# Performance work log

Hardware: AMD Instinct MI355X
Metric: run time of the kernel (lower is better)

Reference implementation:

```python
import jax, jax.numpy as jnp
import numpy as np

B, L, E, H = 4, 4096, 1024, 16
DH = E // H          # 64 head dim
R, M, P = 1, 8, 16   # quadrature nodes, prf features, poly sketch dim
EPS = 1e-6
C = 2.0 + EPS


def setup_inputs() -> dict:
    key = jax.random.key(0)
    ks = jax.random.split(key, 10)
    x = jax.random.normal(ks[0], (B, L, E), dtype=jnp.float32)
    qkv_w = jax.random.normal(ks[1], (E, 3 * E), dtype=jnp.float32) * 0.02
    qkv_b = jnp.zeros((3 * E,), dtype=jnp.float32)
    out_w = jax.random.normal(ks[2], (E, E), dtype=jnp.float32) * 0.02
    out_b = jnp.zeros((E,), dtype=jnp.float32)
    omega = jax.random.normal(ks[3], (R, H, DH, M), dtype=jnp.float32)
    ts_hash1 = jax.random.randint(ks[4], (DH,), 0, P)
    ts_sign1 = jax.random.randint(ks[5], (DH,), 0, 2) * 2 - 1
    ts_hash2 = jax.random.randint(ks[6], (DH,), 0, P)
    ts_sign2 = jax.random.randint(ks[7], (DH,), 0, 2) * 2 - 1
    # laggauss(1): node=1.0, weight=1.0
    quad_nodes = jnp.array([1.0], dtype=jnp.float32) / C
    quad_weights = jnp.array([1.0], dtype=jnp.float32) / C
    return {"x": x, "qkv_w": qkv_w, "qkv_b": qkv_b, "out_w": out_w,
            "out_b": out_b, "omega": omega, "quad_nodes": quad_nodes,
            "quad_weights": quad_weights, "ts_hash1": ts_hash1,
            "ts_sign1": ts_sign1, "ts_hash2": ts_hash2, "ts_sign2": ts_sign2}


def _safe_normalize(x, eps=1e-6):
    norm = jnp.linalg.norm(x, axis=-1, keepdims=True)
    return x / jnp.clip(norm, eps)


def _count_sketch(x, h, s):
    # x: (B,H,L,DH); h,s: (DH,) int
    vals = x * s.astype(x.dtype)
    Mhot = jax.nn.one_hot(h, P, dtype=x.dtype)  # (DH, P)
    return jnp.dot(vals, Mhot)                  # (B,H,L,P)


def _poly_tensor_sketch(x, h1, s1, h2, s2):
    cs1 = _count_sketch(x, h1, s1)
    cs2 = _count_sketch(x, h2, s2)
    f1 = jnp.fft.rfft(cs1, axis=-1)
    f2 = jnp.fft.rfft(cs2, axis=-1)
    ts = jnp.fft.irfft(f1 * f2, n=P, axis=-1)
    return ts / jnp.sqrt(float(P))


def _prf_features(x, omega, quad_nodes):
    proj = jnp.einsum('bhld,rhdm->rbhlm', x, omega)
    s_vals = quad_nodes.reshape(-1, 1, 1, 1, 1)
    sqrt_2s = jnp.sqrt(2.0 * jnp.clip(s_vals, 0.0))
    exp_arg = jnp.clip(proj * sqrt_2s - s_vals, -10.0, 10.0)
    return jnp.exp(exp_arg) / jnp.sqrt(float(M))


def reference(x, qkv_w, qkv_b, out_w, out_b, omega, quad_nodes, quad_weights,
              ts_hash1, ts_sign1, ts_hash2, ts_sign2):
    qkv = x @ qkv_w + qkv_b
    q, k, v = jnp.split(qkv, 3, axis=-1)
    q = q.reshape(B, L, H, DH).transpose(0, 2, 1, 3)
    k = k.reshape(B, L, H, DH).transpose(0, 2, 1, 3)
    v = v.reshape(B, L, H, DH).transpose(0, 2, 1, 3)

    q_norm = _safe_normalize(q)
    k_norm = _safe_normalize(k)

    q_poly = _poly_tensor_sketch(q_norm, ts_hash1, ts_sign1, ts_hash2, ts_sign2)
    k_poly = _poly_tensor_sketch(k_norm, ts_hash1, ts_sign1, ts_hash2, ts_sign2)
    q_prf = _prf_features(q_norm, omega, quad_nodes)
    k_prf = _prf_features(k_norm, omega, quad_nodes)

    sq_w = jnp.sqrt(jnp.clip(quad_weights.reshape(-1, 1, 1, 1, 1), 0.0))
    q_prf = q_prf * sq_w
    k_prf = k_prf * sq_w

    q_fuse = jnp.einsum('bhlp,rbhlm->bhlrpm', q_poly, q_prf).reshape(B, H, L, -1)
    k_fuse = jnp.einsum('bhlp,rbhlm->bhlrpm', k_poly, k_prf).reshape(B, H, L, -1)

    kv = jnp.einsum('bhlf,bhld->bhfd', k_fuse, v)
    context = jnp.einsum('bhlf,bhfd->bhld', q_fuse, kv)
    k_sum = k_fuse.sum(axis=2)                              # (B,H,F)
    norm = jnp.einsum('bhlf,bhf->bhl', q_fuse, k_sum)
    output = context / jnp.clip(norm, 0.0001)[..., None]

    output = output.transpose(0, 2, 1, 3).reshape(B, L, E)
    return output @ out_w + out_b
```

## Files before the change

### kernel.cpp

```cpp
#include <hip/hip_runtime.h>

typedef unsigned short u16;
typedef __attribute__((ext_vector_type(8))) short bfrag8;
typedef __attribute__((ext_vector_type(4))) float f32x4;

__device__ __forceinline__ float b2f(u16 u){ union { unsigned ui; float f; } v; v.ui = ((unsigned)u) << 16; return v.f; }
__device__ __forceinline__ u16 f2b(float f){ union { float f; unsigned ui; } v; v.f = f; unsigned r = (v.ui + 0x7FFF + ((v.ui >> 16) & 1)) >> 16; return (u16)r; }

__device__ __forceinline__ void gl_lds16(const u16* g, u16* l){
  __builtin_amdgcn_global_load_lds(
      (const __attribute__((address_space(1))) unsigned*)g,
      (__attribute__((address_space(3))) unsigned*)l, 16, 0, 0);
}

__global__ __launch_bounds__(256) void zero_f32(float* p, int n){
  int i = blockIdx.x*256 + threadIdx.x;
  if (i < n) p[i] = 0.f;
}

__global__ __launch_bounds__(256) void split_x(const float* __restrict__ x,
    u16* __restrict__ xh, u16* __restrict__ xl){
  size_t i = ((size_t)blockIdx.x*256 + threadIdx.x) * 8;
  float v[8];
  *(float4*)v       = *(const float4*)(x + i);
  *(float4*)(v + 4) = *(const float4*)(x + i + 4);
  u16 h[8], l[8];
  #pragma unroll
  for (int j = 0; j < 8; ++j){ u16 a = f2b(v[j]); h[j] = a; l[j] = f2b(v[j] - b2f(a)); }
  *(uint4*)(xh + i) = *(uint4*)h;
  *(uint4*)(xl + i) = *(uint4*)l;
}

__global__ __launch_bounds__(256) void transpose_split(const float* __restrict__ W,
    u16* __restrict__ Th, u16* __restrict__ Tl, int K, int N){
  __shared__ float tile[32][33];
  int bx = blockIdx.x * 32, by = blockIdx.y * 32;
  int tx = threadIdx.x & 31, ty = threadIdx.x >> 5;
  #pragma unroll
  for (int i = 0; i < 32; i += 8) tile[ty+i][tx] = W[(size_t)(by+ty+i)*N + bx+tx];
  __syncthreads();
  #pragma unroll
  for (int i = 0; i < 32; i += 8){
    float v = tile[tx][ty+i];
    u16 h = f2b(v);
    Th[(size_t)(bx+ty+i)*K + by+tx] = h;
    Tl[(size_t)(bx+ty+i)*K + by+tx] = f2b(v - b2f(h));
  }
}

__global__ __launch_bounds__(256) void transpose_f2b(const float* __restrict__ W, u16* __restrict__ Wt, int K, int N){
  __shared__ u16 tile[32][33];
  int bx = blockIdx.x * 32, by = blockIdx.y * 32;
  int tx = threadIdx.x & 31, ty = threadIdx.x >> 5;
  #pragma unroll
  for (int i = 0; i < 32; i += 8) tile[ty+i][tx] = f2b(W[(size_t)(by+ty+i)*N + bx+tx]);
  __syncthreads();
  #pragma unroll
  for (int i = 0; i < 32; i += 8) Wt[(size_t)(bx+ty+i)*K + by+tx] = tile[tx][ty+i];
}

template<int NPROD>
__global__ __launch_bounds__(256) void gemm_planes(
    const u16* __restrict__ Ah, const u16* __restrict__ Al, int lda,
    const u16* __restrict__ Bh, const u16* __restrict__ Bl, int bn_off,
    const float* __restrict__ bias,
    float* __restrict__ Cq, float* __restrict__ Ck, u16* __restrict__ Cv, int K)
{
  constexpr int NS = (NPROD==3) ? 2 : 1;
  __shared__ __align__(16) u16 As[2*NS*4096];
  __shared__ __align__(16) u16 Bs[2*NS*4096];
  int tid = threadIdx.x, lane = tid & 63, wave = tid >> 6;
  int wm = wave >> 1, wn = wave & 1;
  int bm = blockIdx.y * 128, bn = blockIdx.x * 128;
  f32x4 acc[4][4];
  #pragma unroll
  for (int i=0;i<4;i++)
    #pragma unroll
    for (int j=0;j<4;j++)
      #pragma unroll
      for (int r=0;r<4;r++) acc[i][j][r] = 0.f;
  int mr = lane & 15, g = lane >> 4;
  int srow = (wave & 1)*64 + lane;
  int kc1 = (wave >> 1)*8;
  int kc2 = kc1 + 16;
  const u16* gA0 = Ah + (size_t)(bm + srow)*lda;
  const u16* gA1 = Al + (size_t)(bm + srow)*lda;
  const u16* gB0 = Bh + (size_t)(bn_off + bn + srow)*K;
  const u16* gB1 = Bl + (size_t)(bn_off + bn + srow)*K;
  u16* As0 = As;  u16* As1 = As + NS*4096;
  u16* Bs0 = Bs;  u16* Bs1 = Bs + NS*4096;

#define STG_P(AD, BD, KO) { \
    gl_lds16(gA0 + (KO) + kc1, (AD) + wave*512); \
    gl_lds16(gA0 + (KO) + kc2, (AD) + (wave+4)*512); \
    gl_lds16(gB0 + (KO) + kc1, (BD) + wave*512); \
    gl_lds16(gB0 + (KO) + kc2, (BD) + (wave+4)*512); \
    if constexpr (NS > 1){ \
      gl_lds16(gA1 + (KO) + kc1, (AD) + 4096 + wave*512); \
      gl_lds16(gA1 + (KO) + kc2, (AD) + 4096 + (wave+4)*512); \
      gl_lds16(gB1 + (KO) + kc1, (BD) + 4096 + wave*512); \
      gl_lds16(gB1 + (KO) + kc2, (BD) + 4096 + (wave+4)*512); } }

#define MMACC(sa,sb) \
    { _Pragma("unroll") for (int i=0;i<4;i++){ _Pragma("unroll") for (int j=0;j<4;j++){ \
        acc[i][j] = __builtin_amdgcn_mfma_f32_16x16x32_bf16(af[sa][i], bf[sb][j], acc[i][j], 0, 0, 0); } } }

#define CMP_P(AS, BS) { \
    bfrag8 af[NS][4], bf[NS][4]; \
    _Pragma("unroll") \
    for (int s=0;s<NS;s++){ \
      _Pragma("unroll") \
      for (int i=0;i<4;i++) af[s][i] = *(const bfrag8*)((AS) + s*4096 + g*1024 + (wm*64 + i*16 + mr)*8); \
      _Pragma("unroll") \
      for (int j=0;j<4;j++) bf[s][j] = *(const bfrag8*)((BS) + s*4096 + g*1024 + (wn*64 + j*16 + mr)*8); } \
    if constexpr (NPROD == 3){ MMACC(0,1) MMACC(1,0) } \
    MMACC(0,0) }

  STG_P(As0, Bs0, 0)
  __syncthreads();
  for (int k0 = 0; k0 < K; k0 += 64) {
    STG_P(As1, Bs1, k0 + 32)
    CMP_P(As0, Bs0)
    __syncthreads();
    if (k0 + 64 < K) { STG_P(As0, Bs0, k0 + 64) }
    CMP_P(As1, Bs1)
    __syncthreads();
  }
#undef STG_P
#undef CMP_P
#undef MMACC

  #pragma unroll
  for (int i=0;i<4;i++){
    #pragma unroll
    for (int j=0;j<4;j++){
      int col = bn_off + bn + wn*64 + j*16 + (lane & 15);
      float bv = bias[col];
      #pragma unroll
      for (int r=0;r<4;r++){
        int row = bm + wm*64 + i*16 + (lane>>4)*4 + r;
        float val = acc[i][j][r] + bv;
        if (col < 1024)      Cq[(size_t)row*1024 + col]        = val;
        else if (col < 2048) Ck[(size_t)row*1024 + (col-1024)] = val;
        else                 Cv[(size_t)row*1024 + (col-2048)] = f2b(val);
      }
    }
  }
}

__global__ __launch_bounds__(256) void gemm_b16(const u16* __restrict__ A, int lda,
    const u16* __restrict__ Bt, const float* __restrict__ bias, float* __restrict__ C, int N, int K)
{
  __shared__ __align__(16) u16 As[2*4096];
  __shared__ __align__(16) u16 Bs[2*4096];
  int tid = threadIdx.x, lane = tid & 63, wave = tid >> 6;
  int wm = wave >> 1, wn = wave & 1;
  int bm = blockIdx.y * 128, bn = blockIdx.x * 128;
  f32x4 acc[4][4];
  #pragma unroll
  for (int i=0;i<4;i++)
    #pragma unroll
    for (int j=0;j<4;j++)
      #pragma unroll
      for (int r=0;r<4;r++) acc[i][j][r] = 0.f;
  int mr = lane & 15, g = lane >> 4;
  int srow = (wave & 1)*64 + lane;
  int kc1 = (wave >> 1)*8, kc2 = kc1 + 16;
  const u16* gA = A  + (size_t)(bm + srow)*lda;
  const u16* gB = Bt + (size_t)(bn + srow)*K;
  u16* As0 = As;  u16* As1 = As + 4096;
  u16* Bs0 = Bs;  u16* Bs1 = Bs + 4096;

#define STG_B(AD, BD, KO) { \
    gl_lds16(gA + (KO) + kc1, (AD) + wave*512); \
    gl_lds16(gA + (KO) + kc2, (AD) + (wave+4)*512); \
    gl_lds16(gB + (KO) + kc1, (BD) + wave*512); \
    gl_lds16(gB + (KO) + kc2, (BD) + (wave+4)*512); }

#define CMP_B(AS, BS) { \
    bfrag8 af[4], bf[4]; \
    _Pragma("unroll") \
    for (int i=0;i<4;i++) af[i] = *(const bfrag8*)((AS) + g*1024 + (wm*64 + i*16 + mr)*8); \
    _Pragma("unroll") \
    for (int j=0;j<4;j++) bf[j] = *(const bfrag8*)((BS) + g*1024 + (wn*64 + j*16 + mr)*8); \
    _Pragma("unroll") \
    for (int i=0;i<4;i++){ \
      _Pragma("unroll") \
      for (int j=0;j<4;j++) \
        acc[i][j] = __builtin_amdgcn_mfma_f32_16x16x32_bf16(af[i], bf[j], acc[i][j], 0, 0, 0); } }

  STG_B(As0, Bs0, 0)
  __syncthreads();
  for (int k0 = 0; k0 < K; k0 += 64) {
    STG_B(As1, Bs1, k0 + 32)
    CMP_B(As0, Bs0)
    __syncthreads();
    if (k0 + 64 < K) { STG_B(As0, Bs0, k0 + 64) }
    CMP_B(As1, Bs1)
    __syncthreads();
  }
#undef STG_B
#undef CMP_B

  #pragma unroll
  for (int i=0;i<4;i++){
    #pragma unroll
    for (int j=0;j<4;j++){
      int col = bn + wn*64 + j*16 + (lane & 15);
      float bv = bias[col];
      #pragma unroll
      for (int r=0;r<4;r++){
        int row = bm + wm*64 + i*16 + (lane>>4)*4 + r;
        C[(size_t)row*N + col] = acc[i][j][r] + bv;
      }
    }
  }
}

struct __align__(16) ConsT { int b1; float sg1; int b2; float sg2; };

#define FEATS_COMPUTE(TILE, TOKA)                                                \
  float sq = 0.f;                                                                \
  _Pragma("unroll")                                                              \
  for (int dd = 0; dd < 16; ++dd){ float u = TILE[(TOKA)*65 + g*16 + dd]; sq += u*u; } \
  sq += __shfl_xor(sq, 16); sq += __shfl_xor(sq, 32);                            \
  float sc = 1.f / fmaxf(sqrtf(sq), 1e-6f);                                      \
  float cs1[16], cs2[16], pm[8];                                                 \
  _Pragma("unroll") for (int p=0;p<16;p++){ cs1[p]=0.f; cs2[p]=0.f; }            \
  _Pragma("unroll") for (int m=0;m<8;m++) pm[m]=0.f;                             \
  _Pragma("unroll")                                                              \
  for (int dd = 0; dd < 16; ++dd){                                               \
    int d = g*16 + dd;                                                           \
    float un = TILE[(TOKA)*65 + d] * sc;                                         \
    ConsT cc = cons[d];                                                          \
    float v1 = un*cc.sg1, v2 = un*cc.sg2;                                        \
    _Pragma("unroll")                                                            \
    for (int p=0;p<16;p++){ cs1[p] += (cc.b1==p)?v1:0.f; cs2[p] += (cc.b2==p)?v2:0.f; } \
    _Pragma("unroll")                                                            \
    for (int m=0;m<8;m++) pm[m] += un * oms[d*8 + m];                            \
  }                                                                              \
  _Pragma("unroll")                                                              \
  for (int p=0;p<16;p++){ cs1[p] += __shfl_xor(cs1[p],16); cs1[p] += __shfl_xor(cs1[p],32); \
                          cs2[p] += __shfl_xor(cs2[p],16); cs2[p] += __shfl_xor(cs2[p],32); } \
  _Pragma("unroll")                                                              \
  for (int m=0;m<8;m++){ pm[m] += __shfl_xor(pm[m],16); pm[m] += __shfl_xor(pm[m],32); } \
  float poly4[4];                                                                \
  _Pragma("unroll")                                                              \
  for (int pi=0;pi<4;pi++){ int p = g*4 + pi; float s = 0.f;                     \
    _Pragma("unroll") for (int a=0;a<16;a++) s += cs1[a]*cs2[(p-a)&15];          \
    poly4[pi] = s * 0.25f; }                                                     \
  float prf[8];                                                                  \
  _Pragma("unroll")                                                              \
  for (int m=0;m<8;m++){ float e = fminf(fmaxf(pm[m]*sqrt2s - s_node, -10.f), 10.f); \
    prf[m] = expf(e) * pscale; }

__global__ __launch_bounds__(256) void kfeat_kv(const float* __restrict__ kf, const u16* __restrict__ vb,
    const float* __restrict__ omega, const float* __restrict__ qn, const float* __restrict__ qw,
    const int* __restrict__ h1, const int* __restrict__ s1,
    const int* __restrict__ h2, const int* __restrict__ s2,
    float* __restrict__ kvT, float* __restrict__ ksum)
{
  __shared__ float ktile[64*65];
  __shared__ __align__(16) u16 vtile[64*64];
  __shared__ __align__(16) u16 featT[128*72];
  __shared__ float oms[64*8];
  __shared__ ConsT cons[64];
  int tid = threadIdx.x, lane = tid & 63, wave = tid >> 6;
  int bh = blockIdx.y, b = bh >> 4, h = bh & 15;
  int chunk = blockIdx.x;
  if (tid < 64) {
    ConsT c; c.b1 = h1[tid]; c.sg1 = (float)s1[tid]; c.b2 = h2[tid]; c.sg2 = (float)s2[tid];
    cons[tid] = c;
  }
  for (int i = tid; i < 512; i += 256) oms[i] = omega[h*512 + i];
  float s_node = qn[0];
  float sqrt2s = sqrtf(2.f * fmaxf(s_node, 0.f));
  float pscale = 0.35355339059327373f * sqrtf(fmaxf(qw[0], 0.f));
  int tloc = lane & 15, g = lane >> 4;
  int tokA = wave*16 + tloc;
  int wm = wave >> 1, wn = wave & 1;
  int mr = lane & 15, kq8 = (lane >> 4) * 8;
  f32x4 acc[4][2];
  #pragma unroll
  for (int i=0;i<4;i++)
    #pragma unroll
    for (int jn=0;jn<2;jn++)
      #pragma unroll
      for (int r=0;r<4;r++) acc[i][jn][r] = 0.f;
  float kacc[32];
  #pragma unroll
  for (int j=0;j<32;j++) kacc[j] = 0.f;
  for (int sub = 0; sub < 8; ++sub) {
    int base = chunk*512 + sub*64;
    __syncthreads();
    for (int idx = tid; idx < 4096; idx += 256) {
      int t = idx >> 6, d = idx & 63;
      ktile[t*65 + d] = kf[(size_t)(b*4096 + base + t)*1024 + h*64 + d];
    }
    for (int slot = tid; slot < 512; slot += 256) {
      int t = slot >> 3, o = (slot & 7) * 8;
      *(uint4*)(&vtile[t*64 + o]) = *(const uint4*)(&vb[(size_t)(b*4096 + base + t)*1024 + h*64 + o]);
    }
    __syncthreads();
    {
      FEATS_COMPUTE(ktile, tokA)
      #pragma unroll
      for (int pi=0;pi<4;pi++){
        #pragma unroll
        for (int m=0;m<8;m++){
          int f = (g*4 + pi)*8 + m;
          float v = poly4[pi]*prf[m];
          featT[f*72 + tokA] = f2b(v);
          v += __shfl_xor(v,1); v += __shfl_xor(v,2); v += __shfl_xor(v,4); v += __shfl_xor(v,8);
          if (tloc == 0) kacc[pi*8 + m] += v;
        }
      }
    }
    __syncthreads();
    #pragma unroll
    for (int k0 = 0; k0 < 64; k0 += 32) {
      bfrag8 af[4];
      #pragma unroll
      for (int i=0;i<4;i++) af[i] = *(const bfrag8*)(&featT[(wm*64 + i*16 + mr)*72 + k0 + kq8]);
      #pragma unroll
      for (int jn=0;jn<2;jn++){
        int d = wn*32 + jn*16 + mr;
        short tmp[8];
        #pragma unroll
        for (int j=0;j<8;j++) tmp[j] = (short)vtile[(k0 + kq8 + j)*64 + d];
        bfrag8 bf = *(bfrag8*)tmp;
        #pragma unroll
        for (int i=0;i<4;i++)
          acc[i][jn] = __builtin_amdgcn_mfma_f32_16x16x32_bf16(af[i], bf, acc[i][jn], 0, 0, 0);
      }
    }
  }
  #pragma unroll
  for (int i=0;i<4;i++){
    #pragma unroll
    for (int jn=0;jn<2;jn++){
      int d = wn*32 + jn*16 + (lane & 15);
      #pragma unroll
      for (int r=0;r<4;r++){
        int f = wm*64 + i*16 + (lane>>4)*4 + r;
        atomicAdd(&kvT[((size_t)bh*64 + d)*128 + f], acc[i][jn][r]);
      }
    }
  }
  if (tloc == 0){
    #pragma unroll
    for (int j=0;j<32;j++) atomicAdd(&ksum[bh*128 + g*32 + j], kacc[j]);
  }
}

__global__ __launch_bounds__(256) void qfeat_ctx(const float* __restrict__ qf,
    const float* __restrict__ omega, const float* __restrict__ qn, const float* __restrict__ qw,
    const int* __restrict__ h1, const int* __restrict__ s1,
    const int* __restrict__ h2, const int* __restrict__ s2,
    const float* __restrict__ kvT, const float* __restrict__ ksum,
    u16* __restrict__ attn)
{
  __shared__ float qtile[64*65];
  __shared__ __align__(16) u16 feat[64*136];
  __shared__ __align__(16) u16 kvsb0[64*136];
  __shared__ __align__(16) u16 kvsb1[64*136];
  __shared__ float ksums[128];
  __shared__ float nrm_s[64];
  __shared__ float oms[64*8];
  __shared__ ConsT cons[64];
  int tid = threadIdx.x, lane = tid & 63, wave = tid >> 6;
  int bh = blockIdx.y, b = bh >> 4, h = bh & 15;
  int chunk = blockIdx.x;
  if (tid < 64) {
    ConsT c; c.b1 = h1[tid]; c.sg1 = (float)s1[tid]; c.b2 = h2[tid]; c.sg2 = (float)s2[tid];
    cons[tid] = c;
  }
  for (int i = tid; i < 512; i += 256) oms[i] = omega[h*512 + i];
  for (int idx = tid; idx < 8192; idx += 256) {
    int d = idx >> 7, f = idx & 127;
    float v = kvT[((size_t)bh*64 + d)*128 + f];
    u16 b0 = f2b(v);
    kvsb0[d*136 + f] = b0;
    kvsb1[d*136 + f] = f2b(v - b2f(b0));
  }
  if (tid < 128) ksums[tid] = ksum[bh*128 + tid];
  float s_node = qn[0];
  float sqrt2s = sqrtf(2.f * fmaxf(s_node, 0.f));
  float pscale = 0.35355339059327373f * sqrtf(fmaxf(qw[0], 0.f));
  int tloc = lane & 15, g = lane >> 4;
  int tokA = wave*16 + tloc;
  int mr = lane & 15, kq8 = (lane >> 4) * 8;
  for (int sub = 0; sub < 8; ++sub) {
    int base = chunk*512 + sub*64;
    for (int idx = tid; idx < 4096; idx += 256) {
      int t = idx >> 6, d = idx & 63;
      qtile[t*65 + d] = qf[(size_t)(b*4096 + base + t)*1024 + h*64 + d];
    }
    __syncthreads();
    {
      FEATS_COMPUTE(qtile, tokA)
      float nv = 0.f;
      #pragma unroll
      for (int pi=0;pi<4;pi++){
        #pragma unroll
        for (int m=0;m<8;m++){
          int f = (g*4 + pi)*8 + m;
          float v = poly4[pi]*prf[m];
          feat[tokA*136 + f] = f2b(v);
          nv += v * ksums[f];
        }
      }
      nv += __shfl_xor(nv, 16); nv += __shfl_xor(nv, 32);
      if (lane < 16) nrm_s[tokA] = nv;
    }
    __syncthreads();
    f32x4 cacc[4];
    #pragma unroll
    for (int jn=0;jn<4;jn++)
      #pragma unroll
      for (int r=0;r<4;r++) cacc[jn][r] = 0.f;
    #pragma unroll
    for (int k0 = 0; k0 < 128; k0 += 32) {
      bfrag8 af = *(const bfrag8*)(&feat[(wave*16 + mr)*136 + k0 + kq8]);
      #pragma unroll
      for (int jn=0;jn<4;jn++){
        int d = jn*16 + mr;
        bfrag8 b0 = *(const bfrag8*)(&kvsb0[d*136 + k0 + kq8]);
        cacc[jn] = __builtin_amdgcn_mfma_f32_16x16x32_bf16(af, b0, cacc[jn], 0, 0, 0);
        bfrag8 b1 = *(const bfrag8*)(&kvsb1[d*136 + k0 + kq8]);
        cacc[jn] = __builtin_amdgcn_mfma_f32_16x16x32_bf16(af, b1, cacc[jn], 0, 0, 0);
      }
    }
    #pragma unroll
    for (int jn=0;jn<4;jn++){
      int d = jn*16 + (lane & 15);
      #pragma unroll
      for (int r=0;r<4;r++){
        int row = (lane>>4)*4 + r;
        float nrm = nrm_s[wave*16 + row];
        int tok = base + wave*16 + row;
        attn[(size_t)(b*4096 + tok)*2048 + h*64 + d] = f2b(cacc[jn][r] / fmaxf(nrm, 1e-4f));
      }
    }
  }
}

extern "C" void kernel_launch(void* const* d_in, const int* in_sizes, int n_in,
                              void* d_out, int out_size, void* d_ws, size_t ws_size,
                              hipStream_t stream)
{
  const float* x     = (const float*)d_in[0];
  const float* qkv_w = (const float*)d_in[1];
  const float* qkv_b = (const float*)d_in[2];
  const float* out_w = (const float*)d_in[3];
  const float* out_b = (const float*)d_in[4];
  const float* omega = (const float*)d_in[5];
  const float* qn    = (const float*)d_in[6];
  const float* qw    = (const float*)d_in[7];
  const int* h1 = (const int*)d_in[8];
  const int* s1 = (const int*)d_in[9];
  const int* h2 = (const int*)d_in[10];
  const int* s2 = (const int*)d_in[11];

  const size_t SZ_Q  = (size_t)16384*1024*4;
  const size_t SZ_K  = (size_t)16384*1024*4;
  const size_t SZ_V  = (size_t)16384*1024*2;
  const size_t SZ_XH = (size_t)16384*1024*2;
  const size_t SZ_XL = (size_t)16384*1024*2;
  const size_t SZ_WH = (size_t)3072*1024*2;
  const size_t SZ_WL = (size_t)3072*1024*2;
  const size_t SZ_W2 = (size_t)1024*1024*2;
  const size_t SZ_KV = (size_t)64*64*128*4;
  char* ws = (char*)d_ws;
  float* qf  = (float*)ws;
  float* kf  = (float*)(ws + SZ_Q);
  u16*   vb  = (u16*)  (ws + SZ_Q + SZ_K);
  u16*   xh  = (u16*)  (ws + SZ_Q + SZ_K + SZ_V);
  u16*   xl  = (u16*)  (ws + SZ_Q + SZ_K + SZ_V + SZ_XH);
  u16*   wTh = (u16*)  (ws + SZ_Q + SZ_K + SZ_V + SZ_XH + SZ_XL);
  u16*   wTl = (u16*)  (ws + SZ_Q + SZ_K + SZ_V + SZ_XH + SZ_XL + SZ_WH);
  u16*   wT2 = (u16*)  (ws + SZ_Q + SZ_K + SZ_V + SZ_XH + SZ_XL + SZ_WH + SZ_WL);
  float* kvT = (float*)(ws + SZ_Q + SZ_K + SZ_V + SZ_XH + SZ_XL + SZ_WH + SZ_WL + SZ_W2);
  float* ksp = (float*)(ws + SZ_Q + SZ_K + SZ_V + SZ_XH + SZ_XL + SZ_WH + SZ_WL + SZ_W2 + SZ_KV);

  int nz = (int)((SZ_KV + (size_t)64*128*4) / 4);
  zero_f32<<<(nz+255)/256, 256, 0, stream>>>(kvT, nz);
  split_x<<<(16384*1024/8)/256, 256, 0, stream>>>(x, xh, xl);
  transpose_split<<<dim3(3072/32, 1024/32), 256, 0, stream>>>(qkv_w, wTh, wTl, 1024, 3072);
  transpose_f2b<<<dim3(1024/32, 1024/32), 256, 0, stream>>>(out_w, wT2, 1024, 1024);
  gemm_planes<3><<<dim3(16, 128), 256, 0, stream>>>(xh, xl, 1024, wTh, wTl, 0, qkv_b, qf, kf, vb, 1024);
  gemm_planes<1><<<dim3(8, 128), 256, 0, stream>>>(xh, xl, 1024, wTh, wTl, 2048, qkv_b, qf, kf, vb, 1024);
  kfeat_kv<<<dim3(8, 64), 256, 0, stream>>>(kf, vb, omega, qn, qw, h1, s1, h2, s2, kvT, ksp);
  qfeat_ctx<<<dim3(8, 64), 256, 0, stream>>>(qf, omega, qn, qw, h1, s1, h2, s2, kvT, ksp, (u16*)kf);
  gemm_b16<<<dim3(8, 128), 256, 0, stream>>>((const u16*)kf, 2048, wT2, out_b, (float*)d_out, 1024, 1024);
}
```

Measured before the change: 1.117 ms.

## Overlap next-tile global loads with MFMA using partial vmcnt waits

After: 981.2 us. 12.2% less time.

```diff
diff --git a/kernel.cpp b/kernel.cpp
--- a/kernel.cpp
+++ b/kernel.cpp
@@ -60,7 +60,7 @@
 }
 
 template<int NPROD>
-__global__ __launch_bounds__(256) void gemm_planes(
+__global__ __launch_bounds__(256, (NPROD==3)?2:3) void gemm_planes(
     const u16* __restrict__ Ah, const u16* __restrict__ Al, int lda,
     const u16* __restrict__ Bh, const u16* __restrict__ Bl, int bn_off,
     const float* __restrict__ bias,
@@ -87,47 +87,55 @@
   const u16* gA1 = Al + (size_t)(bm + srow)*lda;
   const u16* gB0 = Bh + (size_t)(bn_off + bn + srow)*K;
   const u16* gB1 = Bl + (size_t)(bn_off + bn + srow)*K;
-  u16* As0 = As;  u16* As1 = As + NS*4096;
-  u16* Bs0 = Bs;  u16* Bs1 = Bs + NS*4096;
-
-#define STG_P(AD, BD, KO) { \
-    gl_lds16(gA0 + (KO) + kc1, (AD) + wave*512); \
-    gl_lds16(gA0 + (KO) + kc2, (AD) + (wave+4)*512); \
-    gl_lds16(gB0 + (KO) + kc1, (BD) + wave*512); \
-    gl_lds16(gB0 + (KO) + kc2, (BD) + (wave+4)*512); \
+
+#define STG(BUF, KO) { \
+    u16* aB = As + (BUF)*NS*4096;  u16* bB = Bs + (BUF)*NS*4096; \
+    gl_lds16(gA0 + (KO) + kc1, aB + wave*512); \
+    gl_lds16(gA0 + (KO) + kc2, aB + (wave+4)*512); \
+    gl_lds16(gB0 + (KO) + kc1, bB + wave*512); \
+    gl_lds16(gB0 + (KO) + kc2, bB + (wave+4)*512); \
     if constexpr (NS > 1){ \
-      gl_lds16(gA1 + (KO) + kc1, (AD) + 4096 + wave*512); \
-      gl_lds16(gA1 + (KO) + kc2, (AD) + 4096 + (wave+4)*512); \
-      gl_lds16(gB1 + (KO) + kc1, (BD) + 4096 + wave*512); \
-      gl_lds16(gB1 + (KO) + kc2, (BD) + 4096 + (wave+4)*512); } }
+      gl_lds16(gA1 + (KO) + kc1, aB + 4096 + wave*512); \
+      gl_lds16(gA1 + (KO) + kc2, aB + 4096 + (wave+4)*512); \
+      gl_lds16(gB1 + (KO) + kc1, bB + 4096 + wave*512); \
+      gl_lds16(gB1 + (KO) + kc2, bB + 4096 + (wave+4)*512); } }
 
 #define MMACC(sa,sb) \
     { _Pragma("unroll") for (int i=0;i<4;i++){ _Pragma("unroll") for (int j=0;j<4;j++){ \
         acc[i][j] = __builtin_amdgcn_mfma_f32_16x16x32_bf16(af[sa][i], bf[sb][j], acc[i][j], 0, 0, 0); } } }
 
-#define CMP_P(AS, BS) { \
+#define CMP(BUF) { \
+    const u16* aB = As + (BUF)*NS*4096;  const u16* bB = Bs + (BUF)*NS*4096; \
     bfrag8 af[NS][4], bf[NS][4]; \
     _Pragma("unroll") \
     for (int s=0;s<NS;s++){ \
       _Pragma("unroll") \
-      for (int i=0;i<4;i++) af[s][i] = *(const bfrag8*)((AS) + s*4096 + g*1024 + (wm*64 + i*16 + mr)*8); \
+      for (int i=0;i<4;i++) af[s][i] = *(const bfrag8*)(aB + s*4096 + g*1024 + (wm*64 + i*16 + mr)*8); \
       _Pragma("unroll") \
-      for (int j=0;j<4;j++) bf[s][j] = *(const bfrag8*)((BS) + s*4096 + g*1024 + (wn*64 + j*16 + mr)*8); } \
+      for (int j=0;j<4;j++) bf[s][j] = *(const bfrag8*)(bB + s*4096 + g*1024 + (wn*64 + j*16 + mr)*8); } \
     if constexpr (NPROD == 3){ MMACC(0,1) MMACC(1,0) } \
     MMACC(0,0) }
 
-  STG_P(As0, Bs0, 0)
-  __syncthreads();
-  for (int k0 = 0; k0 < K; k0 += 64) {
-    STG_P(As1, Bs1, k0 + 32)
-    CMP_P(As0, Bs0)
-    __syncthreads();
-    if (k0 + 64 < K) { STG_P(As0, Bs0, k0 + 64) }
-    CMP_P(As1, Bs1)
-    __syncthreads();
-  }
-#undef STG_P
-#undef CMP_P
+  STG(0, 0)
+  int cur = 0;
+  for (int k0 = 0; k0 < K - 32; k0 += 32) {
+    STG(cur^1, k0 + 32)
+    if constexpr (NS > 1) asm volatile("s_waitcnt vmcnt(8)" ::: "memory");
+    else                  asm volatile("s_waitcnt vmcnt(4)" ::: "memory");
+    __builtin_amdgcn_sched_barrier(0);
+    __builtin_amdgcn_s_barrier();
+    __builtin_amdgcn_sched_barrier(0);
+    CMP(cur)
+    __builtin_amdgcn_s_barrier();
+    cur ^= 1;
+  }
+  asm volatile("s_waitcnt vmcnt(0)" ::: "memory");
+  __builtin_amdgcn_sched_barrier(0);
+  __builtin_amdgcn_s_barrier();
+  __builtin_amdgcn_sched_barrier(0);
+  CMP(cur)
+#undef STG
+#undef CMP
 #undef MMACC
 
   #pragma unroll
@@ -148,7 +156,7 @@
   }
 }
 
-__global__ __launch_bounds__(256) void gemm_b16(const u16* __restrict__ A, int lda,
+__global__ __launch_bounds__(256, 3) void gemm_b16(const u16* __restrict__ A, int lda,
     const u16* __restrict__ Bt, const float* __restrict__ bias, float* __restrict__ C, int N, int K)
 {
   __shared__ __align__(16) u16 As[2*4096];
@@ -168,37 +176,44 @@
   int kc1 = (wave >> 1)*8, kc2 = kc1 + 16;
   const u16* gA = A  + (size_t)(bm + srow)*lda;
   const u16* gB = Bt + (size_t)(bn + srow)*K;
-  u16* As0 = As;  u16* As1 = As + 4096;
-  u16* Bs0 = Bs;  u16* Bs1 = Bs + 4096;
-
-#define STG_B(AD, BD, KO) { \
-    gl_lds16(gA + (KO) + kc1, (AD) + wave*512); \
-    gl_lds16(gA + (KO) + kc2, (AD) + (wave+4)*512); \
-    gl_lds16(gB + (KO) + kc1, (BD) + wave*512); \
-    gl_lds16(gB + (KO) + kc2, (BD) + (wave+4)*512); }
-
-#define CMP_B(AS, BS) { \
+
+#define STG_B(BUF, KO) { \
+    u16* aB = As + (BUF)*4096;  u16* bB = Bs + (BUF)*4096; \
+    gl_lds16(gA + (KO) + kc1, aB + wave*512); \
+    gl_lds16(gA + (KO) + kc2, aB + (wave+4)*512); \
+    gl_lds16(gB + (KO) + kc1, bB + wave*512); \
+    gl_lds16(gB + (KO) + kc2, bB + (wave+4)*512); }
+
+#define CMP_B(BUF) { \
+    const u16* aB = As + (BUF)*4096;  const u16* bB = Bs + (BUF)*4096; \
     bfrag8 af[4], bf[4]; \
     _Pragma("unroll") \
-    for (int i=0;i<4;i++) af[i] = *(const bfrag8*)((AS) + g*1024 + (wm*64 + i*16 + mr)*8); \
+    for (int i=0;i<4;i++) af[i] = *(const bfrag8*)(aB + g*1024 + (wm*64 + i*16 + mr)*8); \
     _Pragma("unroll") \
-    for (int j=0;j<4;j++) bf[j] = *(const bfrag8*)((BS) + g*1024 + (wn*64 + j*16 + mr)*8); \
+    for (int j=0;j<4;j++) bf[j] = *(const bfrag8*)(bB + g*1024 + (wn*64 + j*16 + mr)*8); \
     _Pragma("unroll") \
     for (int i=0;i<4;i++){ \
       _Pragma("unroll") \
       for (int j=0;j<4;j++) \
         acc[i][j] = __builtin_amdgcn_mfma_f32_16x16x32_bf16(af[i], bf[j], acc[i][j], 0, 0, 0); } }
 
-  STG_B(As0, Bs0, 0)
-  __syncthreads();
-  for (int k0 = 0; k0 < K; k0 += 64) {
-    STG_B(As1, Bs1, k0 + 32)
-    CMP_B(As0, Bs0)
-    __syncthreads();
-    if (k0 + 64 < K) { STG_B(As0, Bs0, k0 + 64) }
-    CMP_B(As1, Bs1)
-    __syncthreads();
-  }
+  STG_B(0, 0)
+  int cur = 0;
+  for (int k0 = 0; k0 < K - 32; k0 += 32) {
+    STG_B(cur^1, k0 + 32)
+    asm volatile("s_waitcnt vmcnt(4)" ::: "memory");
+    __builtin_amdgcn_sched_barrier(0);
+    __builtin_amdgcn_s_barrier();
+    __builtin_amdgcn_sched_barrier(0);
+    CMP_B(cur)
+    __builtin_amdgcn_s_barrier();
+    cur ^= 1;
+  }
+  asm volatile("s_waitcnt vmcnt(0)" ::: "memory");
+  __builtin_amdgcn_sched_barrier(0);
+  __builtin_amdgcn_s_barrier();
+  __builtin_amdgcn_sched_barrier(0);
+  CMP_B(cur)
 #undef STG_B
 #undef CMP_B
 
```
